# Performance work log

Hardware: AMD Instinct MI355X
Metric: run time of the kernel (lower is better)

Reference implementation:

```python
import jax, jax.numpy as jnp
import numpy as np
import math

NUM_HEADS = 16
ROPE_BASE = 10000.0


def _rope_cos_sin(seq_len, head_dim, dtype):
    # Qwen2-style rotary embeddings. The torch source builds cos/sin of width
    # head_dim by concatenating freqs with itself, so the first and second
    # halves are identical; the half-width table below is the equivalent math.
    half = head_dim // 2
    inv_freq = 1.0 / (ROPE_BASE ** (jnp.arange(0, head_dim, 2, dtype=jnp.float32) / head_dim))
    t = jnp.arange(seq_len, dtype=jnp.float32)
    freqs = jnp.einsum('i,j->ij', t, inv_freq)  # [S, half]
    cos = jnp.cos(freqs).astype(dtype)[None, None]  # [1,1,S,half]
    sin = jnp.sin(freqs).astype(dtype)[None, None]
    return cos, sin


def _apply_rope(x, cos, sin):
    # x: [B, H, S, D]; split-half rotation (Qwen2 rotate-half convention)
    half = x.shape[-1] // 2
    x1, x2 = x[..., :half], x[..., half:]
    return jnp.concatenate([x1 * cos - x2 * sin, x2 * cos + x1 * sin], axis=-1)


def setup_inputs() -> dict:
    key = jax.random.key(0)
    ks = jax.random.split(key, 5)
    B, S, H = 2, 2048, 2048
    scale = 1.0 / math.sqrt(H)
    return {
        'hidden_states': jax.random.normal(ks[0], (B, S, H), dtype=jnp.float32),
        'Wq': jax.random.normal(ks[1], (H, H), dtype=jnp.float32) * scale,
        'Wk': jax.random.normal(ks[2], (H, H), dtype=jnp.float32) * scale,
        'Wv': jax.random.normal(ks[3], (H, H), dtype=jnp.float32) * scale,
        'Wo': jax.random.normal(ks[4], (H, H), dtype=jnp.float32) * scale,
    }


def reference(hidden_states, Wq, Wk, Wv, Wo):
    B, S, H = hidden_states.shape
    nh = NUM_HEADS
    hd = H // nh

    def proj(W):
        # nn.Linear: x @ W.T ; then [B,S,H] -> [B,nh,S,hd]
        y = jnp.einsum('bsh,oh->bso', hidden_states, W)
        return y.reshape(B, S, nh, hd).transpose(0, 2, 1, 3)

    q, k, v = proj(Wq), proj(Wk), proj(Wv)

    cos, sin = _rope_cos_sin(S, hd, hidden_states.dtype)
    q = _apply_rope(q, cos, sin)
    k = _apply_rope(k, cos, sin)

    scores = jnp.einsum('bhqd,bhkd->bhqk', q, k) / math.sqrt(hd)
    causal = jnp.triu(jnp.full((S, S), -jnp.inf, dtype=scores.dtype), k=1)
    scores = scores + causal[None, None]
    probs = jax.nn.softmax(scores, axis=-1)

    ctx = jnp.einsum('bhqk,bhkd->bhqd', probs, v)  # [B,nh,S,hd]
    ctx = ctx.transpose(0, 2, 1, 3).reshape(B, S, H)
    out = jnp.einsum('bsh,oh->bso', ctx, Wo)
    return out
```

## Files before the change

### kernel.cpp

```cpp
#include <hip/hip_runtime.h>

#define S_LEN 2048
#define HID   2048
#define NHEAD 16
#define HD    128
#define BSZ   2
#define BS_TOT (BSZ * S_LEN)
#define QKS   4096

typedef __bf16 bf16x8 __attribute__((ext_vector_type(8)));
typedef unsigned short u16x8 __attribute__((ext_vector_type(8)));
typedef unsigned short u16x4 __attribute__((ext_vector_type(4)));
typedef float f32x4 __attribute__((ext_vector_type(4)));

static __device__ __forceinline__ bf16x8 as_bf(u16x8 v) { return __builtin_bit_cast(bf16x8, v); }

static __device__ __forceinline__ unsigned short f2bf(float f) {
  __bf16 h = (__bf16)f;
  return __builtin_bit_cast(unsigned short, h);
}
static __device__ __forceinline__ float bf2f(unsigned short b) {
  unsigned int u = ((unsigned int)b) << 16;
  return __builtin_bit_cast(float, u);
}

static __device__ __forceinline__ void gload_lds16(const unsigned short* g, unsigned short* l) {
  __builtin_amdgcn_global_load_lds((const __attribute__((address_space(1))) unsigned int*)g,
                                   (__attribute__((address_space(3))) unsigned int*)l, 16, 0, 0);
}

__global__ __launch_bounds__(256) void cvt_all(const float* __restrict__ hs,
                                               const float* __restrict__ Wq,
                                               const float* __restrict__ Wk,
                                               const float* __restrict__ Wv,
                                               const float* __restrict__ Wo,
                                               unsigned short* __restrict__ hsb,
                                               unsigned short* __restrict__ wall,
                                               float* __restrict__ ct, float* __restrict__ st) {
  int b = (int)blockIdx.x, tid = (int)threadIdx.x;
  if (b < 8192) {
    int i = b * 256 + tid;
    float4 v = ((const float4*)hs)[i];
    ushort4 o; o.x = f2bf(v.x); o.y = f2bf(v.y); o.z = f2bf(v.z); o.w = f2bf(v.w);
    ((ushort4*)hsb)[i] = o;
  } else if (b < 24576) {
    int t = b - 8192;
    int wsel = t >> 12;
    const float* in = (wsel == 0) ? Wq : (wsel == 1) ? Wk : (wsel == 2) ? Wv : Wo;
    int i = (t & 4095) * 256 + tid;
    float4 v = ((const float4*)in)[i];
    ushort4 o; o.x = f2bf(v.x); o.y = f2bf(v.y); o.z = f2bf(v.z); o.w = f2bf(v.w);
    ((ushort4*)(wall + (size_t)wsel * HID * HID))[i] = o;
  } else {
    int id = (b - 24576) * 256 + tid;
    int tt = id >> 6, d = id & 63;
    float inv = powf(10000.0f, -(float)d * (1.0f / 64.0f));
    float f = (float)tt * inv;
    float sv, cv;
    sincosf(f, &sv, &cv);
    ct[id] = cv; st[id] = sv;
  }
}

__global__ __launch_bounds__(256) void rope_apply_k(unsigned short* __restrict__ qk,
                                                    const float* __restrict__ ct,
                                                    const float* __restrict__ st) {
  int id = blockIdx.x * 256 + threadIdx.x;
  int d4 = (id & 15) * 4;
  int h = (id >> 4) & (NHEAD - 1);
  int m = id >> 8;
  int s = m & (S_LEN - 1);
  float4 c  = *(const float4*)(ct + s * 64 + d4);
  float4 sn = *(const float4*)(st + s * 64 + d4);
  size_t base = (size_t)m * QKS + 2048 + h * HD + d4;
  u16x4 k1 = *(u16x4*)(qk + base), k2 = *(u16x4*)(qk + base + 64);
  u16x4 p1, p2;
  float cc[4] = {c.x, c.y, c.z, c.w}, ss[4] = {sn.x, sn.y, sn.z, sn.w};
#pragma unroll
  for (int j = 0; j < 4; ++j) {
    float ak = bf2f(k1[j]), bk = bf2f(k2[j]);
    p1[j] = f2bf(ak * cc[j] - bk * ss[j]);
    p2[j] = f2bf(bk * cc[j] + ak * ss[j]);
  }
  *(u16x4*)(qk + base) = p1;
  *(u16x4*)(qk + base + 64) = p2;
}

template <typename OutT>
__global__ __launch_bounds__(512, 1) void gemm256(const unsigned short* __restrict__ A,
                                                  const unsigned short* __restrict__ Bw,
                                                  OutT* __restrict__ C, int M, int N, int K) {
  __shared__ __align__(16) unsigned short As[2][256 * 64];
  __shared__ __align__(16) unsigned short Bs[2][256 * 64];
  int x = (int)blockIdx.x;
  int chunk = (int)gridDim.x >> 3;
  int x2 = (x & 7) * chunk + (x >> 3);
  const int nbn = N >> 8;
  int bm = x2 / nbn, bn = x2 % nbn;
  int tid = (int)threadIdx.x;
  int l = tid & 63, lr = l & 15, lg = l >> 4;
  int w = tid >> 6;
  int wm = w >> 2, wn = w & 3;

  int arow0 = wm * 128 + 8 * (w & 3) + (l >> 3);
  int brow0 = 8 * w + (l >> 3);
  int sslot = ((l & 7) ^ (l >> 3)) * 8;
  const unsigned short* gAb = A + (size_t)(bm * 256 + arow0) * K + sslot;
  const unsigned short* gBb = Bw + (size_t)(bn * 256 + brow0) * K + sslot;

  int arw = (wm * 128 + lr) * 64;
  int brw = (wn * 64 + lr) * 64;
  int acol0 = ((0 + lg) ^ (lr & 7)) * 8;
  int acol1 = ((4 + lg) ^ (lr & 7)) * 8;

  f32x4 zero = {0.f, 0.f, 0.f, 0.f};
  f32x4 acc[8][4];
#pragma unroll
  for (int mi = 0; mi < 8; ++mi)
#pragma unroll
    for (int ni = 0; ni < 4; ++ni) acc[mi][ni] = zero;

  int nk = K >> 6;
  int nk2 = nk >> 1;

#define ISSUE_A(buf, tile, c)                                                  \
  gload_lds16(gAb + (size_t)(32 * (c)) * K + (tile) * 64,                      \
              &As[buf][8192 * wm + 2048 * (c) + 512 * (w & 3)])
#define ISSUE_B(buf, tile, c)                                                  \
  gload_lds16(gBb + (size_t)(64 * (c)) * K + (tile) * 64,                      \
              &Bs[buf][4096 * (c) + 512 * w])
#define HT(buf, tile, c)                                                       \
  do { ISSUE_B(buf, tile, c); ISSUE_A(buf, tile, c); } while (0)
#define VM6 asm volatile("s_waitcnt vmcnt(6)" ::: "memory")

#define LOADB(d)                                                               \
  do {                                                                         \
    _Pragma("unroll") for (int ni = 0; ni < 4; ++ni) {                         \
      bfr[ni][0] = *(const u16x8*)&Bs[d][brw + ni * 1024 + acol0];             \
      bfr[ni][1] = *(const u16x8*)&Bs[d][brw + ni * 1024 + acol1];             \
    }                                                                          \
  } while (0)

#define PHASE(d, q, LASTW, ...)                                                \
  do {                                                                         \
    u16x8 paf[2][2];                                                           \
    _Pragma("unroll") for (int m2 = 0; m2 < 2; ++m2) {                         \
      paf[m2][0] = *(const u16x8*)&As[d][arw + ((q) * 2 + m2) * 1024 + acol0]; \
      paf[m2][1] = *(const u16x8*)&As[d][arw + ((q) * 2 + m2) * 1024 + acol1]; \
    }                                                                          \
    __VA_ARGS__;                                                               \
    __builtin_amdgcn_sched_barrier(0);                                         \
    __builtin_amdgcn_s_barrier();                                              \
    __builtin_amdgcn_s_setprio(1);                                             \
    _Pragma("unroll") for (int m2 = 0; m2 < 2; ++m2)                           \
      _Pragma("unroll") for (int ni = 0; ni < 4; ++ni) {                       \
        acc[(q) * 2 + m2][ni] = __builtin_amdgcn_mfma_f32_16x16x32_bf16(       \
            as_bf(paf[m2][0]), as_bf(bfr[ni][0]), acc[(q) * 2 + m2][ni], 0, 0, 0); \
        acc[(q) * 2 + m2][ni] = __builtin_amdgcn_mfma_f32_16x16x32_bf16(       \
            as_bf(paf[m2][1]), as_bf(bfr[ni][1]), acc[(q) * 2 + m2][ni], 0, 0, 0); \
      }                                                                        \
    __builtin_amdgcn_s_setprio(0);                                             \
    LASTW;                                                                     \
    __builtin_amdgcn_s_barrier();                                              \
  } while (0)

  HT(0, 0, 0); HT(0, 0, 1); HT(0, 0, 2); HT(0, 0, 3);
  HT(1, 1, 0); HT(1, 1, 1); HT(1, 1, 2);
  VM6;
  __builtin_amdgcn_s_barrier();

  for (int t = 0; t < nk2; ++t) {
    int Todd = 2 * t + 1;
    int T2 = (2 * t + 2) & (nk - 1);
    int T3 = (2 * t + 3) & (nk - 1);
    u16x8 bfr[4][2];
    LOADB(0);
    PHASE(0, 0, (void)0, HT(1, Todd, 3));
    PHASE(0, 1, (void)0, HT(0, T2, 0));
    PHASE(0, 2, (void)0, HT(0, T2, 1));
    PHASE(0, 3, VM6,     HT(0, T2, 2));
    LOADB(1);
    PHASE(1, 0, (void)0, HT(0, T2, 3));
    PHASE(1, 1, (void)0, HT(1, T3, 0));
    PHASE(1, 2, (void)0, HT(1, T3, 1));
    PHASE(1, 3, VM6,     HT(1, T3, 2));
  }
#undef PHASE
#undef LOADB
#undef VM6
#undef HT
#undef ISSUE_A
#undef ISSUE_B

#pragma unroll
  for (int mi = 0; mi < 8; ++mi) {
#pragma unroll
    for (int ni = 0; ni < 4; ++ni) {
      int col = bn * 256 + wn * 64 + ni * 16 + lr;
#pragma unroll
      for (int j = 0; j < 4; ++j) {
        int rowm = bm * 256 + wm * 128 + mi * 16 + 4 * lg + j;
        float v = acc[mi][ni][j];
        if constexpr (sizeof(OutT) == 2) C[(size_t)rowm * N + col] = f2bf(v);
        else                             C[(size_t)rowm * N + col] = v;
      }
    }
  }
  (void)M;
}

template <typename OutT>
__global__ __launch_bounds__(256) void gemm128(const unsigned short* __restrict__ A,
                                               const unsigned short* __restrict__ Bw,
                                               OutT* __restrict__ C, int M, int N, int K) {
  __shared__ __align__(16) unsigned short As[4][128 * 32];
  __shared__ __align__(16) unsigned short Bs[4][128 * 32];
  int x = (int)blockIdx.x;
  int chunk = (int)gridDim.x >> 3;
  int x2 = (x & 7) * chunk + (x >> 3);
  const int nbn = N >> 7;
  int bm = x2 / nbn, bn = x2 % nbn;
  int tid = (int)threadIdx.x;
  int l = tid & 63, lr = l & 15, lg = l >> 4;
  int w = tid >> 6, wm = w >> 1, wn = w & 1;

  int w32 = 32 * w;
  int srow = w32 + (l >> 2);
  int ssw = ((l >> 2) ^ (l >> 4)) & 3;
  const unsigned short* gA = A + (size_t)(bm * 128 + srow) * K + (((l & 3) ^ ssw) << 3);
  const unsigned short* gB = Bw + (size_t)(bn * 128 + srow) * K + (((l & 3) ^ ssw) << 3);

  int rsw = (lr ^ (lr >> 2)) & 3;
  int aoff[4], boff[4];
#pragma unroll
  for (int i = 0; i < 4; ++i) {
    aoff[i] = (wm * 64 + i * 16 + lr) * 32 + ((lg ^ rsw) << 3);
    boff[i] = (wn * 64 + i * 16 + lr) * 32 + ((lg ^ rsw) << 3);
  }

  f32x4 zero = {0.f, 0.f, 0.f, 0.f};
  f32x4 acc[4][4];
#pragma unroll
  for (int mi = 0; mi < 4; ++mi)
#pragma unroll
    for (int ni = 0; ni < 4; ++ni) acc[mi][ni] = zero;

  int nk = K >> 5;

#define STAGE(buf, kt)                                                        \
  do {                                                                        \
    const unsigned short* pa_ = gA + (size_t)(kt) * 32;                       \
    const unsigned short* pb_ = gB + (size_t)(kt) * 32;                       \
    gload_lds16(pa_, &As[buf][w32 * 32]);                                     \
    gload_lds16(pa_ + (size_t)16 * K, &As[buf][(w32 + 16) * 32]);             \
    gload_lds16(pb_, &Bs[buf][w32 * 32]);                                     \
    gload_lds16(pb_ + (size_t)16 * K, &Bs[buf][(w32 + 16) * 32]);             \
  } while (0)

#define COMPUTE(buf)                                                          \
  do {                                                                        \
    u16x8 af[4], bfr[4];                                                      \
    _Pragma("unroll") for (int i = 0; i < 4; ++i) {                           \
      af[i] = *(const u16x8*)&As[buf][aoff[i]];                               \
      bfr[i] = *(const u16x8*)&Bs[buf][boff[i]];                              \
    }                                                                         \
    _Pragma("unroll") for (int mi = 0; mi < 4; ++mi)                          \
        _Pragma("unroll") for (int ni = 0; ni < 4; ++ni)                      \
            acc[mi][ni] = __builtin_amdgcn_mfma_f32_16x16x32_bf16(            \
                as_bf(af[mi]), as_bf(bfr[ni]), acc[mi][ni], 0, 0, 0);         \
  } while (0)

  STAGE(0, 0);
  STAGE(1, 1);
  STAGE(2, 2);
  asm volatile("s_waitcnt vmcnt(8)" ::: "memory");
  __builtin_amdgcn_s_barrier();
#pragma unroll 4
  for (int kt = 0; kt < nk; ++kt) {
    COMPUTE(kt & 3);
    asm volatile("s_waitcnt vmcnt(4) lgkmcnt(0)" ::: "memory");
    __builtin_amdgcn_s_barrier();
    STAGE((kt + 3) & 3, (kt + 3) & (nk - 1));
  }
#undef STAGE
#undef COMPUTE

#pragma unroll
  for (int mi = 0; mi < 4; ++mi) {
#pragma unroll
    for (int ni = 0; ni < 4; ++ni) {
      int col = bn * 128 + wn * 64 + ni * 16 + lr;
#pragma unroll
      for (int j = 0; j < 4; ++j) {
        int rowm = bm * 128 + wm * 64 + mi * 16 + 4 * lg + j;
        float v = acc[mi][ni][j];
        if constexpr (sizeof(OutT) == 2) C[(size_t)rowm * N + col] = f2bf(v);
        else                             C[(size_t)rowm * N + col] = v;
      }
    }
  }
  (void)M;
}

__global__ __launch_bounds__(256, 2) void attn_fwd(const unsigned short* __restrict__ qk,
                                                   const unsigned short* __restrict__ vt,
                                                   unsigned short* __restrict__ ctx,
                                                   const float* __restrict__ ct,
                                                   const float* __restrict__ st) {
  __shared__ __align__(16) unsigned short Ks[2][64 * 128];
  __shared__ __align__(16) unsigned short Vs[2][128 * 64];
  __shared__ __align__(16) unsigned short Ps[4 * 32 * 64];

  int x = (int)blockIdx.x;
  int bh, qt;
  if (x < 256) { bh = x & 31;         qt = 15 - (x >> 5); }
  else         { bh = (x - 256) & 31; qt = (x - 256) >> 5; }
  int b = bh >> 4, h = bh & 15;
  int q0 = qt * 128;
  int nt = 2 * qt + 2;

  int tid = (int)threadIdx.x;
  int w = tid >> 6, l = tid & 63, lr = l & 15, lg = l >> 4;
  const float CEXP = 0.12751744f;
  const float MB   = -23.0831391f;
  const int bS = b * S_LEN, h128 = h * HD;
  const int qw = q0 + w * 32;
  const unsigned short* qg = qk;
  const unsigned short* kg = qk + 2048;

  u16x8 qfr[2][4];
#pragma unroll
  for (int qf = 0; qf < 2; ++qf) {
    const unsigned short* qb = qg + (size_t)(bS + qw + qf * 16 + lr) * QKS + h128;
#pragma unroll
    for (int kk = 0; kk < 4; ++kk) qfr[qf][kk] = *(const u16x8*)(qb + kk * 32 + lg * 8);
    int spos = qw + qf * 16 + lr;
#pragma unroll
    for (int kk = 0; kk < 2; ++kk) {
      int d0 = kk * 32 + lg * 8;
      float4 c0 = *(const float4*)(ct + spos * 64 + d0);
      float4 c1 = *(const float4*)(ct + spos * 64 + d0 + 4);
      float4 s0 = *(const float4*)(st + spos * 64 + d0);
      float4 s1 = *(const float4*)(st + spos * 64 + d0 + 4);
      float cc[8] = {c0.x, c0.y, c0.z, c0.w, c1.x, c1.y, c1.z, c1.w};
      float sv[8] = {s0.x, s0.y, s0.z, s0.w, s1.x, s1.y, s1.z, s1.w};
      u16x8 lo = qfr[qf][kk], hi = qfr[qf][kk + 2];
#pragma unroll
      for (int j = 0; j < 8; ++j) {
        float a = bf2f(lo[j]), b2 = bf2f(hi[j]);
        lo[j] = f2bf(a * cc[j] - b2 * sv[j]);
        hi[j] = f2bf(b2 * cc[j] + a * sv[j]);
      }
      qfr[qf][kk] = lo; qfr[qf][kk + 2] = hi;
    }
  }

  const unsigned short* kbg[4];
  const unsigned short* vbg[4];
#pragma unroll
  for (int i = 0; i < 4; ++i) {
    int rr = 16 * w + 4 * i + (l >> 4);
    int colK = ((l & 15) ^ (rr & 15)) * 8;
    kbg[i] = kg + (size_t)(bS + rr) * QKS + h128 + colK;
    int vd = 32 * w + 8 * i + (l >> 3);
    int colV = ((l & 7) ^ (vd & 7)) * 8;
    vbg[i] = vt + (size_t)(h128 + vd) * BS_TOT + bS + colV;
  }

#define ASTAGE(buf, t)                                                        \
  do {                                                                        \
    size_t koff_ = (size_t)(t) * 64 * QKS;                                    \
    int voff_ = (t) * 64;                                                     \
    _Pragma("unroll") for (int i_ = 0; i_ < 4; ++i_) {                        \
      gload_lds16(kbg[i_] + koff_, &Ks[buf][(16 * w + 4 * i_) * 128]);        \
      gload_lds16(vbg[i_] + voff_, &Vs[buf][(32 * w + 8 * i_) * 64]);         \
    }                                                                         \
  } while (0)

  f32x4 zero = {0.f, 0.f, 0.f, 0.f};
  f32x4 oacc[2][8];
#pragma unroll
  for (int qf = 0; qf < 2; ++qf)
#pragma unroll
    for (int nj = 0; nj < 8; ++nj) oacc[qf][nj] = zero;
  float lsum[2] = {0.f, 0.f};

  int cur = 0;
  ASTAGE(0, 0);
  __syncthreads();

  for (int t = 0; t < nt; ++t) {
    int k0 = t * 64;
    if (t + 1 < nt) ASTAGE(cur ^ 1, t + 1);

    if (k0 <= qw + 31) {
      const unsigned short* KsB = &Ks[cur][0];
      const unsigned short* VsB = &Vs[cur][0];

      f32x4 sac[2][4];
#pragma unroll
      for (int qf = 0; qf < 2; ++qf)
#pragma unroll
        for (int ni = 0; ni < 4; ++ni) sac[qf][ni] = zero;
      __builtin_amdgcn_s_setprio(1);
#pragma unroll
      for (int kk = 0; kk < 4; ++kk) {
#pragma unroll
        for (int ni = 0; ni < 4; ++ni) {
          u16x8 kf = *(const u16x8*)&KsB[(ni * 16 + lr) * 128 + (((kk * 4 + lg) ^ lr) * 8)];
          sac[0][ni] = __builtin_amdgcn_mfma_f32_16x16x32_bf16(as_bf(kf), as_bf(qfr[0][kk]), sac[0][ni], 0, 0, 0);
          sac[1][ni] = __builtin_amdgcn_mfma_f32_16x16x32_bf16(as_bf(kf), as_bf(qfr[1][kk]), sac[1][ni], 0, 0, 0);
        }
      }
      __builtin_amdgcn_s_setprio(0);

      u16x8 vfr[2][8];
#pragma unroll
      for (int kk2 = 0; kk2 < 2; ++kk2)
#pragma unroll
        for (int nj = 0; nj < 8; ++nj)
          vfr[kk2][nj] = *(const u16x8*)&VsB[(nj * 16 + lr) * 64 + (((kk2 * 4 + lg) ^ (lr & 7)) * 8)];

      bool needmask = (k0 + 63 > qw);
      unsigned short* pw = &Ps[w * 2048];

#pragma unroll
      for (int qf = 0; qf < 2; ++qf) {
        float s[4][4];
#pragma unroll
        for (int ni = 0; ni < 4; ++ni)
#pragma unroll
          for (int j = 0; j < 4; ++j) s[ni][j] = sac[qf][ni][j];
        if (needmask) {
          int qgl = qw + qf * 16 + lr;
#pragma unroll
          for (int ni = 0; ni < 4; ++ni)
#pragma unroll
            for (int j = 0; j < 4; ++j)
              if (k0 + ni * 16 + 4 * lg + j > qgl) s[ni][j] = -1e30f;
        }
        float rs = 0.f;
#pragma unroll
        for (int ni = 0; ni < 4; ++ni)
#pragma unroll
          for (int j = 0; j < 4; ++j) {
            float p = exp2f(fmaf(s[ni][j], CEXP, MB));
            s[ni][j] = p; rs += p;
          }
        lsum[qf] += rs;
#pragma unroll
        for (int ni = 0; ni < 4; ++ni) {
          u16x4 pv = {f2bf(s[ni][0]), f2bf(s[ni][1]), f2bf(s[ni][2]), f2bf(s[ni][3])};
          *(u16x4*)&pw[(qf * 16 + lr) * 64 + (((2 * ni + (lg >> 1)) ^ (lr & 7)) * 8) + (lg & 1) * 4] = pv;
        }
        __builtin_amdgcn_s_setprio(1);
#pragma unroll
        for (int kk2 = 0; kk2 < 2; ++kk2) {
          u16x8 pa = *(const u16x8*)&pw[(qf * 16 + lr) * 64 + (((kk2 * 4 + lg) ^ (lr & 7)) * 8)];
#pragma unroll
          for (int nj = 0; nj < 8; ++nj)
            oacc[qf][nj] = __builtin_amdgcn_mfma_f32_16x16x32_bf16(as_bf(pa), as_bf(vfr[kk2][nj]), oacc[qf][nj], 0, 0, 0);
        }
        __builtin_amdgcn_s_setprio(0);
      }
    }

    __syncthreads();
    cur ^= 1;
  }
#undef ASTAGE

#pragma unroll
  for (int qf = 0; qf < 2; ++qf) {
    float ls = lsum[qf];
    ls += __shfl_xor(ls, 16);
    ls += __shfl_xor(ls, 32);
    float rl = 1.0f / ls;
    float r0 = __shfl(rl, 4 * lg + 0, 16);
    float r1 = __shfl(rl, 4 * lg + 1, 16);
    float r2 = __shfl(rl, 4 * lg + 2, 16);
    float r3 = __shfl(rl, 4 * lg + 3, 16);
    size_t obase = (size_t)(bS + qw + qf * 16 + 4 * lg) * HID + h128;
#pragma unroll
    for (int nj = 0; nj < 8; ++nj) {
      ctx[obase + 0 * HID + nj * 16 + lr] = f2bf(oacc[qf][nj][0] * r0);
      ctx[obase + 1 * HID + nj * 16 + lr] = f2bf(oacc[qf][nj][1] * r1);
      ctx[obase + 2 * HID + nj * 16 + lr] = f2bf(oacc[qf][nj][2] * r2);
      ctx[obase + 3 * HID + nj * 16 + lr] = f2bf(oacc[qf][nj][3] * r3);
    }
  }
}

extern "C" void kernel_launch(void* const* d_in, const int* in_sizes, int n_in,
                              void* d_out, int out_size, void* d_ws, size_t ws_size,
                              hipStream_t stream) {
  const float* hs = (const float*)d_in[0];
  const float* Wq = (const float*)d_in[1];
  const float* Wk = (const float*)d_in[2];
  const float* Wv = (const float*)d_in[3];
  const float* Wo = (const float*)d_in[4];

  char* ws = (char*)d_ws;
  unsigned short* hsb  = (unsigned short*)(ws);
  unsigned short* wall = (unsigned short*)(ws + 16777216);
  unsigned short* qkb  = (unsigned short*)(ws + 50331648);
  unsigned short* vtb  = (unsigned short*)(ws + 83886080);
  float* ctab = (float*)(ws + 100663296);
  float* stab = (float*)(ws + 101187584);
  unsigned short* ctxb = hsb;

  cvt_all<<<25088, 256, 0, stream>>>(hs, Wq, Wk, Wv, Wo, hsb, wall, ctab, stab);

  gemm256<unsigned short><<<256, 512, 0, stream>>>(hsb, wall, qkb, BS_TOT, 2 * HID, HID);
  gemm128<unsigned short><<<512, 256, 0, stream>>>(wall + 2 * (size_t)HID * HID, hsb, vtb, HID, BS_TOT, HID);

  rope_apply_k<<<4096, 256, 0, stream>>>(qkb, ctab, stab);

  attn_fwd<<<512, 256, 0, stream>>>(qkb, vtb, ctxb, ctab, stab);

  gemm128<float><<<512, 256, 0, stream>>>(ctxb, wall + 3 * (size_t)HID * HID, (float*)d_out, BS_TOT, HID, HID);

  (void)in_sizes; (void)n_in; (void)out_size; (void)ws_size;
}
```

Baseline: 263.6 us.

## Split long causal attention tiles across two blocks and merge with a combine kernel

The eight longest query tiles per head (qt 8–15) are each split into two key ranges handled by separate blocks. Each block writes a normalized partial output and its row sum to workspace memory that is no longer needed. A new combine kernel blends the two halves by their row sums, which is valid because the softmax uses a fixed max offset. The aim is better load balance across the causal triangle. K/V staging drops from double to single buffering with an extra barrier, so LDS shrinks and the launch bound rises to three blocks per CU. The cost is less load/compute overlap, an extra launch, and extra memory traffic for the partial results.

```diff
diff --git a/kernel.cpp b/kernel.cpp
--- a/kernel.cpp
+++ b/kernel.cpp
@@ -302,22 +302,39 @@
   (void)M;
 }
 
-__global__ __launch_bounds__(256, 2) void attn_fwd(const unsigned short* __restrict__ qk,
+__global__ __launch_bounds__(256, 3) void attn_fwd(const unsigned short* __restrict__ qk,
                                                    const unsigned short* __restrict__ vt,
                                                    unsigned short* __restrict__ ctx,
                                                    const float* __restrict__ ct,
-                                                   const float* __restrict__ st) {
-  __shared__ __align__(16) unsigned short Ks[2][64 * 128];
-  __shared__ __align__(16) unsigned short Vs[2][128 * 64];
+                                                   const float* __restrict__ st,
+                                                   unsigned short* __restrict__ pO,
+                                                   float* __restrict__ pls) {
+  __shared__ __align__(16) unsigned short Ks[64 * 128];
+  __shared__ __align__(16) unsigned short Vs[128 * 64];
   __shared__ __align__(16) unsigned short Ps[4 * 32 * 64];
 
   int x = (int)blockIdx.x;
-  int bh, qt;
-  if (x < 256) { bh = x & 31;         qt = 15 - (x >> 5); }
-  else         { bh = (x - 256) & 31; qt = (x - 256) >> 5; }
+  int bh, qt, half, tile0, ntL;
+  bool split;
+  if (x < 512) {
+    split = true;
+    bh = x & 31;
+    int pair = x >> 5;
+    qt = 15 - (pair >> 1);
+    half = pair & 1;
+    ntL = qt + 1;
+    tile0 = half * ntL;
+  } else {
+    split = false;
+    int i = x - 512;
+    bh = i & 31;
+    qt = 7 - (i >> 5);
+    half = 0;
+    ntL = 2 * qt + 2;
+    tile0 = 0;
+  }
   int b = bh >> 4, h = bh & 15;
   int q0 = qt * 128;
-  int nt = 2 * qt + 2;
 
   int tid = (int)threadIdx.x;
   int w = tid >> 6, l = tid & 63, lr = l & 15, lg = l >> 4;
@@ -367,13 +384,13 @@
     vbg[i] = vt + (size_t)(h128 + vd) * BS_TOT + bS + colV;
   }
 
-#define ASTAGE(buf, t)                                                        \
+#define ASTAGE(t)                                                             \
   do {                                                                        \
     size_t koff_ = (size_t)(t) * 64 * QKS;                                    \
     int voff_ = (t) * 64;                                                     \
     _Pragma("unroll") for (int i_ = 0; i_ < 4; ++i_) {                        \
-      gload_lds16(kbg[i_] + koff_, &Ks[buf][(16 * w + 4 * i_) * 128]);        \
-      gload_lds16(vbg[i_] + voff_, &Vs[buf][(32 * w + 8 * i_) * 64]);         \
+      gload_lds16(kbg[i_] + koff_, &Ks[(16 * w + 4 * i_) * 128]);             \
+      gload_lds16(vbg[i_] + voff_, &Vs[(32 * w + 8 * i_) * 64]);              \
     }                                                                         \
   } while (0)
 
@@ -385,19 +402,17 @@
     for (int nj = 0; nj < 8; ++nj) oacc[qf][nj] = zero;
   float lsum[2] = {0.f, 0.f};
 
-  int cur = 0;
-  ASTAGE(0, 0);
+  ASTAGE(tile0);
   __syncthreads();
 
-  for (int t = 0; t < nt; ++t) {
+  for (int tl = 0; tl < ntL; ++tl) {
+    int t = tile0 + tl;
     int k0 = t * 64;
-    if (t + 1 < nt) ASTAGE(cur ^ 1, t + 1);
-
-    if (k0 <= qw + 31) {
-      const unsigned short* KsB = &Ks[cur][0];
-      const unsigned short* VsB = &Vs[cur][0];
-
-      f32x4 sac[2][4];
+    bool active = (k0 <= qw + 31);
+
+    f32x4 sac[2][4];
+    u16x8 vfr[2][8];
+    if (active) {
 #pragma unroll
       for (int qf = 0; qf < 2; ++qf)
 #pragma unroll
@@ -407,23 +422,25 @@
       for (int kk = 0; kk < 4; ++kk) {
 #pragma unroll
         for (int ni = 0; ni < 4; ++ni) {
-          u16x8 kf = *(const u16x8*)&KsB[(ni * 16 + lr) * 128 + (((kk * 4 + lg) ^ lr) * 8)];
+          u16x8 kf = *(const u16x8*)&Ks[(ni * 16 + lr) * 128 + (((kk * 4 + lg) ^ lr) * 8)];
           sac[0][ni] = __builtin_amdgcn_mfma_f32_16x16x32_bf16(as_bf(kf), as_bf(qfr[0][kk]), sac[0][ni], 0, 0, 0);
           sac[1][ni] = __builtin_amdgcn_mfma_f32_16x16x32_bf16(as_bf(kf), as_bf(qfr[1][kk]), sac[1][ni], 0, 0, 0);
         }
       }
       __builtin_amdgcn_s_setprio(0);
-
-      u16x8 vfr[2][8];
 #pragma unroll
       for (int kk2 = 0; kk2 < 2; ++kk2)
 #pragma unroll
         for (int nj = 0; nj < 8; ++nj)
-          vfr[kk2][nj] = *(const u16x8*)&VsB[(nj * 16 + lr) * 64 + (((kk2 * 4 + lg) ^ (lr & 7)) * 8)];
-
+          vfr[kk2][nj] = *(const u16x8*)&Vs[(nj * 16 + lr) * 64 + (((kk2 * 4 + lg) ^ (lr & 7)) * 8)];
+    }
+
+    __syncthreads();
+    if (tl + 1 < ntL) ASTAGE(t + 1);
+
+    if (active) {
       bool needmask = (k0 + 63 > qw);
       unsigned short* pw = &Ps[w * 2048];
-
 #pragma unroll
       for (int qf = 0; qf < 2; ++qf) {
         float s[4][4];
@@ -466,7 +483,6 @@
     }
 
     __syncthreads();
-    cur ^= 1;
   }
 #undef ASTAGE
 
@@ -480,15 +496,51 @@
     float r1 = __shfl(rl, 4 * lg + 1, 16);
     float r2 = __shfl(rl, 4 * lg + 2, 16);
     float r3 = __shfl(rl, 4 * lg + 3, 16);
-    size_t obase = (size_t)(bS + qw + qf * 16 + 4 * lg) * HID + h128;
-#pragma unroll
-    for (int nj = 0; nj < 8; ++nj) {
-      ctx[obase + 0 * HID + nj * 16 + lr] = f2bf(oacc[qf][nj][0] * r0);
-      ctx[obase + 1 * HID + nj * 16 + lr] = f2bf(oacc[qf][nj][1] * r1);
-      ctx[obase + 2 * HID + nj * 16 + lr] = f2bf(oacc[qf][nj][2] * r2);
-      ctx[obase + 3 * HID + nj * 16 + lr] = f2bf(oacc[qf][nj][3] * r3);
+    if (!split) {
+      size_t obase = (size_t)(bS + qw + qf * 16 + 4 * lg) * HID + h128;
+#pragma unroll
+      for (int nj = 0; nj < 8; ++nj) {
+        ctx[obase + 0 * HID + nj * 16 + lr] = f2bf(oacc[qf][nj][0] * r0);
+        ctx[obase + 1 * HID + nj * 16 + lr] = f2bf(oacc[qf][nj][1] * r1);
+        ctx[obase + 2 * HID + nj * 16 + lr] = f2bf(oacc[qf][nj][2] * r2);
+        ctx[obase + 3 * HID + nj * 16 + lr] = f2bf(oacc[qf][nj][3] * r3);
+      }
+    } else {
+      int t256 = (qt - 8) * 32 + bh;
+      int rowq = w * 32 + qf * 16 + 4 * lg;
+      size_t pbase = ((size_t)(half * 256 + t256) * 128 + rowq) * 128;
+#pragma unroll
+      for (int nj = 0; nj < 8; ++nj) {
+        pO[pbase + 0 * 128 + nj * 16 + lr] = f2bf(oacc[qf][nj][0] * r0);
+        pO[pbase + 1 * 128 + nj * 16 + lr] = f2bf(oacc[qf][nj][1] * r1);
+        pO[pbase + 2 * 128 + nj * 16 + lr] = f2bf(oacc[qf][nj][2] * r2);
+        pO[pbase + 3 * 128 + nj * 16 + lr] = f2bf(oacc[qf][nj][3] * r3);
+      }
+      if (lg == 0)
+        pls[(half * 256 + t256) * 128 + w * 32 + qf * 16 + lr] = ls;
     }
   }
+}
+
+__global__ __launch_bounds__(256) void combine(const unsigned short* __restrict__ pO,
+                                               const float* __restrict__ pls,
+                                               unsigned short* __restrict__ ctx) {
+  int vid = blockIdx.x * 256 + threadIdx.x;
+  int t = vid >> 11;
+  int rr = (vid >> 4) & 127;
+  int d8 = vid & 15;
+  int qt8 = t >> 5, bh = t & 31, b = bh >> 4, h = bh & 15;
+  float l1 = pls[t * 128 + rr];
+  float l2 = pls[(256 + t) * 128 + rr];
+  float inv = 1.0f / (l1 + l2);
+  float w1 = l1 * inv, w2 = l2 * inv;
+  u16x8 a = *(const u16x8*)&pO[((size_t)t * 128 + rr) * 128 + d8 * 8];
+  u16x8 c = *(const u16x8*)&pO[((size_t)(256 + t) * 128 + rr) * 128 + d8 * 8];
+  u16x8 o;
+#pragma unroll
+  for (int j = 0; j < 8; ++j) o[j] = f2bf(bf2f(a[j]) * w1 + bf2f(c[j]) * w2);
+  size_t obase = (size_t)(b * S_LEN + (qt8 + 8) * 128 + rr) * HID + h * HD + d8 * 8;
+  *(u16x8*)&ctx[obase] = o;
 }
 
 extern "C" void kernel_launch(void* const* d_in, const int* in_sizes, int n_in,
@@ -508,6 +560,8 @@
   float* ctab = (float*)(ws + 100663296);
   float* stab = (float*)(ws + 101187584);
   unsigned short* ctxb = hsb;
+  unsigned short* pO = wall;
+  float* pls = (float*)(ws + 16777216 + 16777216);
 
   cvt_all<<<25088, 256, 0, stream>>>(hs, Wq, Wk, Wv, Wo, hsb, wall, ctab, stab);
 
@@ -516,7 +570,8 @@
 
   rope_apply_k<<<4096, 256, 0, stream>>>(qkb, ctab, stab);
 
-  attn_fwd<<<512, 256, 0, stream>>>(qkb, vtb, ctxb, ctab, stab);
+  attn_fwd<<<768, 256, 0, stream>>>(qkb, vtb, ctxb, ctab, stab, pO, pls);
+  combine<<<2048, 256, 0, stream>>>(pO, pls, ctxb);
 
   gemm128<float><<<512, 256, 0, stream>>>(ctxb, wall + 3 * (size_t)HID * HID, (float*)d_out, BS_TOT, HID, HID);
 
```

Measured after the change: 621.2 us. 136% more time.
